# Kernel tuning notes

Measured on AMD Instinct MI355X. Metric: run time of the kernel, lower is better.

The kernel has to match this reference:

```python
import jax, jax.numpy as jnp
import numpy as np

B, T, C = 2, 4096, 512
H = 8
MEMORY = 256  # window: key j visible to query i iff 0 <= i - j <= MEMORY


def setup_inputs() -> dict:
    key = jax.random.key(0)
    k1, k2, k3 = jax.random.split(key, 3)
    x = jax.random.normal(k1, (B, T, C), dtype=jnp.float32)
    w_attn = jax.random.normal(k2, (3 * C, C), dtype=jnp.float32) * 0.02
    w_proj = jax.random.normal(k3, (C, C), dtype=jnp.float32) * 0.02
    return {"x": x, "w_attn": w_attn, "w_proj": w_proj}


def reference(x, w_attn, w_proj):
    b, t, c = x.shape
    d = c // H
    # fused QKV projection (Linear without bias): x @ W^T
    qkv = jnp.einsum('btc,fc->btf', x, w_attn)  # [B,T,3C]
    q, k, v = jnp.split(qkv, 3, axis=-1)
    # [B,T,C] -> [B,H,T,d]
    q = q.reshape(b, t, H, d).transpose(0, 2, 1, 3)
    k = k.reshape(b, t, H, d).transpose(0, 2, 1, 3)
    v = v.reshape(b, t, H, d).transpose(0, 2, 1, 3)
    # sliding-window causal mask: tril(0) & ~tril(-memory-1)
    i = jnp.arange(t)[:, None]
    j = jnp.arange(t)[None, :]
    mask = (j <= i) & (i - j <= MEMORY)  # [T,T] bool
    scores = jnp.einsum('bhqd,bhkd->bhqk', q, k) * (1.0 / np.sqrt(d))
    scores = jnp.where(mask, scores, -jnp.inf)
    attn = jax.nn.softmax(scores, axis=-1)
    y = jnp.einsum('bhqk,bhkd->bhqd', attn, v)  # [B,H,T,d]
    y = y.transpose(0, 2, 1, 3).reshape(b, t, c)
    # output projection
    y = jnp.einsum('btc,fc->btf', y, w_proj)
    return y
```

## Files before the change

### kernel.cpp

```cpp
#include <hip/hip_runtime.h>
#include <hip/hip_bf16.h>
#include <stdint.h>

#define BB 2
#define TT 4096
#define CC 512
#define HH 8
#define MEM 256

typedef unsigned short u16;
typedef __bf16 bf16x8 __attribute__((ext_vector_type(8)));
typedef float floatx4 __attribute__((ext_vector_type(4)));

__device__ inline u16 f2bf(float f) {
  uint32_t u = __float_as_uint(f);
  uint32_t r = (u + 0x7fffu + ((u >> 16) & 1u)) >> 16;
  return (u16)r;
}
__device__ inline u16 f2bf_r(float f) {
  return (u16)((__float_as_uint(f) + 0x8000u) >> 16);
}

__device__ inline void gld16(const u16* g, u16* lds) {
  __builtin_amdgcn_global_load_lds(
      (const __attribute__((address_space(1))) uint32_t*)g,
      (__attribute__((address_space(3))) uint32_t*)lds, 16, 0, 0);
}

#define BARM() asm volatile("" ::: "memory")

__global__ __launch_bounds__(256) void cvt_all(const float* __restrict__ x,
                                               const float* __restrict__ wa,
                                               const float* __restrict__ wp,
                                               u16* __restrict__ xb,
                                               u16* __restrict__ wab,
                                               u16* __restrict__ wpb) {
  int i = blockIdx.x * 256 + threadIdx.x;
  const float* s; u16* d; int off;
  if (i < 1048576) { s = x; d = xb; off = i; }
  else if (i < 1245184) { s = wa; d = wab; off = i - 1048576; }
  else { s = wp; d = wpb; off = i - 1245184; }
  float4 v = *reinterpret_cast<const float4*>(s + (size_t)off * 4);
  ushort4 o;
  o.x = f2bf(v.x); o.y = f2bf(v.y); o.z = f2bf(v.z); o.w = f2bf(v.w);
  *reinterpret_cast<ushort4*>(d + (size_t)off * 4) = o;
}

__device__ inline void stage_hA(const u16* __restrict__ G, u16* lds, int K,
                                int gr0, int koff, int half, int wv, int lane) {
#pragma unroll
  for (int j = 0; j < 2; j++) {
    int lrow = (j * 8 + wv) * 8 + (lane >> 3);
    int row = (lrow & 63) + ((lrow >> 6) << 7) + (half << 6);
    int blk = (lane & 7) ^ (row & 7);
    gld16(G + (size_t)(gr0 + row) * K + koff + blk * 8,
          lds + (size_t)row * 64 + (lane & 7) * 8);
  }
}
__device__ inline void stage_hB(const u16* __restrict__ G, u16* lds, int K,
                                int gr0, int koff, int half, int wv, int lane) {
  if (half == 0) {
#pragma unroll
    for (int j = 0; j < 2; j++) {
      int lrow = (j * 8 + wv) * 8 + (lane >> 3);
      int row = (lrow & 31) + (lrow >> 5) * 48;
      int blk = (lane & 7) ^ (row & 7);
      gld16(G + (size_t)(gr0 + row) * K + koff + blk * 8,
            lds + (size_t)row * 64 + (lane & 7) * 8);
    }
  } else {
    int lrow = wv * 8 + (lane >> 3);
    int row = 32 + (lrow & 15) + (lrow >> 4) * 48;
    int blk = (lane & 7) ^ (row & 7);
    gld16(G + (size_t)(gr0 + row) * K + koff + blk * 8,
          lds + (size_t)row * 64 + (lane & 7) * 8);
  }
}

#define PHASE(MQ, NQ, NF, STAGE, WAITV)                                        \
  {                                                                            \
    bf16x8 af[4][2], bfv[NF][2];                                               \
    _Pragma("unroll") for (int fm = 0; fm < 4; fm++) {                         \
      int row = wm * 128 + MQ * 64 + fm * 16 + l16;                            \
      const u16* p = Ad + (size_t)row * 64;                                    \
      af[fm][0] = *(const bf16x8*)(p + ((quad ^ (row & 7)) << 3));             \
      af[fm][1] = *(const bf16x8*)(p + (((4 + quad) ^ (row & 7)) << 3));       \
    }                                                                          \
    _Pragma("unroll") for (int fn = 0; fn < NF; fn++) {                        \
      int row = wn * 48 + NQ * 32 + fn * 16 + l16;                             \
      const u16* p = Bd + (size_t)row * 64;                                    \
      bfv[fn][0] = *(const bf16x8*)(p + ((quad ^ (row & 7)) << 3));            \
      bfv[fn][1] = *(const bf16x8*)(p + (((4 + quad) ^ (row & 7)) << 3));      \
    }                                                                          \
    STAGE;                                                                     \
    BARM();                                                                    \
    __builtin_amdgcn_s_barrier();                                              \
    asm volatile("s_waitcnt lgkmcnt(0)" ::: "memory");                         \
    __builtin_amdgcn_sched_barrier(0);                                         \
    __builtin_amdgcn_s_setprio(1);                                             \
    _Pragma("unroll") for (int fm = 0; fm < 4; fm++)                           \
      _Pragma("unroll") for (int fn = 0; fn < NF; fn++) {                      \
        acc[MQ * 4 + fm][NQ * 2 + fn] =                                        \
            __builtin_amdgcn_mfma_f32_16x16x32_bf16(                           \
                af[fm][0], bfv[fn][0], acc[MQ * 4 + fm][NQ * 2 + fn], 0, 0, 0);\
        acc[MQ * 4 + fm][NQ * 2 + fn] =                                        \
            __builtin_amdgcn_mfma_f32_16x16x32_bf16(                           \
                af[fm][1], bfv[fn][1], acc[MQ * 4 + fm][NQ * 2 + fn], 0, 0, 0);\
      }                                                                        \
    __builtin_amdgcn_s_setprio(0);                                             \
    WAITV;                                                                     \
    BARM();                                                                    \
    __builtin_amdgcn_s_barrier();                                              \
    BARM();                                                                    \
  }

__global__ __launch_bounds__(512, 2) void gemm256(const u16* __restrict__ A,
                                                  const u16* __restrict__ Bw,
                                                  u16* __restrict__ C,
                                                  int M, int N, int K) {
  __shared__ __align__(16) u16 As[2][256 * 64];
  __shared__ __align__(16) u16 Bs[2][192 * 64];
  const int tid = threadIdx.x;
  const int lane = tid & 63, wv = tid >> 6;
  const int quad = lane >> 4, l16 = lane & 15;
  const int wm = wv >> 2, wn = wv & 3;

  const int nbx = N / 192;
  const int nwg = (M >> 8) * nbx;
  int wg = blockIdx.x;
  if ((nwg & 7) == 0) wg = (wg & 7) * (nwg >> 3) + (wg >> 3);
  const int m0 = (wg / nbx) << 8, n0 = (wg % nbx) * 192;

  const int nK = K >> 6;
  floatx4 acc[8][3] = {};

  stage_hA(A, As[0], K, m0, 0, 0, wv, lane);
  stage_hA(A, As[0], K, m0, 0, 1, wv, lane);
  stage_hB(Bw, Bs[0], K, n0, 0, 0, wv, lane);
  stage_hB(Bw, Bs[0], K, n0, 0, 1, wv, lane);
  if (nK > 1) {
    stage_hA(A, As[1], K, m0, 64, 0, wv, lane);
    stage_hB(Bw, Bs[1], K, n0, 64, 0, wv, lane);
    asm volatile("s_waitcnt vmcnt(4)" ::: "memory");
  } else {
    asm volatile("s_waitcnt vmcnt(0)" ::: "memory");
  }
  BARM();
  __builtin_amdgcn_s_barrier();
  BARM();

  for (int t = 0; t < nK; ++t) {
    const int d = t & 1;
    u16* Ad = As[d]; u16* Bd = Bs[d];
    u16* An = As[d ^ 1]; u16* Bn = Bs[d ^ 1];
    const int k1 = (t + 1) << 6, k2 = (t + 2) << 6;

    PHASE(0, 0, 2, { if (t + 1 < nK) stage_hA(A, An, K, m0, k1, 1, wv, lane); }, {})
    PHASE(0, 1, 1, { if (t + 1 < nK) stage_hB(Bw, Bn, K, n0, k1, 1, wv, lane); }, {})
    PHASE(1, 0, 2, { if (t + 2 < nK) stage_hA(A, Ad, K, m0, k2, 0, wv, lane); }, {})
    PHASE(1, 1, 1, { if (t + 2 < nK) stage_hB(Bw, Bd, K, n0, k2, 0, wv, lane); },
          { if (t + 2 < nK) asm volatile("s_waitcnt vmcnt(4)" ::: "memory");
            else            asm volatile("s_waitcnt vmcnt(0)" ::: "memory"); })
  }

#pragma unroll
  for (int mi = 0; mi < 8; mi++) {
    int row = m0 + wm * 128 + mi * 16 + quad * 4;
#pragma unroll
    for (int ni = 0; ni < 3; ni++) {
      int col = n0 + wn * 48 + ni * 16 + l16;
#pragma unroll
      for (int r = 0; r < 4; r++)
        C[(size_t)(row + r) * N + col] = f2bf(acc[mi][ni][r]);
    }
  }
}

__global__ __launch_bounds__(256) void gemm_bt_n64(const u16* __restrict__ A,
                                                   const u16* __restrict__ Bw,
                                                   float* __restrict__ C,
                                                   int M, int N, int K) {
  __shared__ __align__(16) u16 As[128 * 32];
  __shared__ __align__(16) u16 Bs[64 * 32];
  const int tid = threadIdx.x;
  const int w = tid >> 6, lane = tid & 63, quad = lane >> 4, l16 = lane & 15;
  const int m0 = blockIdx.x * 128, n0 = blockIdx.y * 64;

  floatx4 acc[2][4] = {};
  const int nK = K >> 5;
  for (int kb = 0; kb < nK; ++kb) {
    const int kof = kb * 32;
    {
      int c = tid;
      gld16(A + (size_t)(m0 + (c >> 2)) * K + kof + (c & 3) * 8, As + (size_t)c * 8);
      c = tid + 256;
      gld16(A + (size_t)(m0 + (c >> 2)) * K + kof + (c & 3) * 8, As + (size_t)c * 8);
      c = tid;
      gld16(Bw + (size_t)(n0 + (c >> 2)) * K + kof + (c & 3) * 8, Bs + (size_t)c * 8);
    }
    __syncthreads();
    bf16x8 af[2], bfr[4];
#pragma unroll
    for (int i = 0; i < 2; i++)
      af[i] = *reinterpret_cast<const bf16x8*>(&As[(w * 32 + i * 16 + l16) * 32 + quad * 8]);
#pragma unroll
    for (int i = 0; i < 4; i++)
      bfr[i] = *reinterpret_cast<const bf16x8*>(&Bs[(i * 16 + l16) * 32 + quad * 8]);
#pragma unroll
    for (int mi = 0; mi < 2; mi++)
#pragma unroll
      for (int ni = 0; ni < 4; ni++)
        acc[mi][ni] = __builtin_amdgcn_mfma_f32_16x16x32_bf16(af[mi], bfr[ni], acc[mi][ni], 0, 0, 0);
    __syncthreads();
  }
#pragma unroll
  for (int mi = 0; mi < 2; mi++) {
    int row = m0 + w * 32 + mi * 16 + quad * 4;
#pragma unroll
    for (int ni = 0; ni < 4; ni++) {
      int col = n0 + ni * 16 + l16;
#pragma unroll
      for (int r = 0; r < 4; r++)
        C[(size_t)(row + r) * N + col] = acc[mi][ni][r];
    }
  }
}

__global__ __launch_bounds__(256, 2) void attn_win(const u16* __restrict__ qkv,
                                                   u16* __restrict__ y) {
  const int q0 = blockIdx.x * 128;
  const int h = blockIdx.y;
  const int b = blockIdx.z;
  const int tid = threadIdx.x;
  const int w = tid >> 6, lane = tid & 63, quad = lane >> 4, l16 = lane & 15;

  __shared__ __align__(16) u16 Qs[128 * 64];
  __shared__ __align__(16) u16 Ks[64 * 64];
  __shared__ __align__(16) u16 Vt[64 * 72];
  __shared__ __align__(16) u16 Ps[4][32 * 72];

  const size_t baseQ = ((size_t)(b * TT + q0)) * 1536 + h * 64;
#pragma unroll
  for (int j = 0; j < 4; j++) {
    int c = tid + j * 256, row = c >> 3, blk = (c & 7) ^ (row & 7);
    gld16(qkv + baseQ + (size_t)row * 1536 + blk * 8, Qs + (size_t)c * 8);
  }
  __syncthreads();
  bf16x8 qf[2][2];
#pragma unroll
  for (int mi = 0; mi < 2; mi++) {
    int row = w * 32 + mi * 16 + l16;
    qf[mi][0] = *reinterpret_cast<const bf16x8*>(&Qs[row * 64 + (quad ^ (l16 & 7)) * 8]);
    qf[mi][1] = *reinterpret_cast<const bf16x8*>(&Qs[row * 64 + ((quad + 4) ^ (l16 & 7)) * 8]);
#pragma unroll
    for (int e = 0; e < 8; e++) {
      qf[mi][0][e] = qf[mi][0][e] * (__bf16)0.125f;
      qf[mi][1][e] = qf[mi][1][e] * (__bf16)0.125f;
    }
  }

  floatx4 acc_o[2][4] = {};
  float l_acc[2][4] = {{0.f, 0.f, 0.f, 0.f}, {0.f, 0.f, 0.f, 0.f}};

  const int s_min = (q0 >= 256) ? 0 : ((256 - q0) >> 6);
  const int key_v = tid >> 3, dc_v = tid & 7;
  const int key_v1 = (tid + 256) >> 3, dc_v1 = tid & 7;

  uint4 vp0, vp1;
  {
    size_t baseV = ((size_t)(b * TT + (q0 - 256 + s_min * 64))) * 1536 + 1024 + h * 64;
    vp0 = *reinterpret_cast<const uint4*>(qkv + baseV + (size_t)key_v * 1536 + dc_v * 8);
    vp1 = *reinterpret_cast<const uint4*>(qkv + baseV + (size_t)key_v1 * 1536 + dc_v1 * 8);
  }

  for (int s = s_min; s < 6; ++s) {
    const int k0 = q0 - 256 + s * 64;
    const size_t baseK = ((size_t)(b * TT + k0)) * 1536 + 512 + h * 64;
    {
      int c = tid, row = c >> 3, blk = (c & 7) ^ (row & 7);
      gld16(qkv + baseK + (size_t)row * 1536 + blk * 8, Ks + (size_t)c * 8);
      c = tid + 256; row = c >> 3; blk = (c & 7) ^ (row & 7);
      gld16(qkv + baseK + (size_t)row * 1536 + blk * 8, Ks + (size_t)c * 8);
    }
    {
      u16 tmp[8];
      *reinterpret_cast<uint4*>(tmp) = vp0;
      int col = key_v ^ (dc_v * 8);
#pragma unroll
      for (int e = 0; e < 8; e++) Vt[(dc_v * 8 + e) * 72 + col] = tmp[e];
      *reinterpret_cast<uint4*>(tmp) = vp1;
      col = key_v1 ^ (dc_v1 * 8);
#pragma unroll
      for (int e = 0; e < 8; e++) Vt[(dc_v1 * 8 + e) * 72 + col] = tmp[e];
    }
    if (s < 5) {
      size_t baseV = ((size_t)(b * TT + k0 + 64)) * 1536 + 1024 + h * 64;
      vp0 = *reinterpret_cast<const uint4*>(qkv + baseV + (size_t)key_v * 1536 + dc_v * 8);
      vp1 = *reinterpret_cast<const uint4*>(qkv + baseV + (size_t)key_v1 * 1536 + dc_v1 * 8);
    }
    __syncthreads();

    int mode = 0;
    if (s == 0) mode = (w < 2) ? 1 : 3;
    else if (s == 1) mode = (w < 2) ? 0 : 1;
    else if (s == 4) mode = (w < 2) ? 2 : 0;
    else if (s == 5) mode = (w < 2) ? 3 : 2;

    if (mode != 3) {
      bf16x8 bfr[4][2];
#pragma unroll
      for (int nt = 0; nt < 4; nt++) {
        int krow = nt * 16 + l16;
        bfr[nt][0] = *reinterpret_cast<const bf16x8*>(&Ks[krow * 64 + (quad ^ (l16 & 7)) * 8]);
        bfr[nt][1] = *reinterpret_cast<const bf16x8*>(&Ks[krow * 64 + ((quad + 4) ^ (l16 & 7)) * 8]);
      }
      floatx4 sc[2][4] = {};
#pragma unroll
      for (int mi = 0; mi < 2; mi++)
#pragma unroll
        for (int nt = 0; nt < 4; nt++) {
          sc[mi][nt] = __builtin_amdgcn_mfma_f32_16x16x32_bf16(qf[mi][0], bfr[nt][0], sc[mi][nt], 0, 0, 0);
          sc[mi][nt] = __builtin_amdgcn_mfma_f32_16x16x32_bf16(qf[mi][1], bfr[nt][1], sc[mi][nt], 0, 0, 0);
        }
      const int hqb = (w & 1) * 32 + quad * 4;
      if (mode == 1) {
#pragma unroll
        for (int mi = 0; mi < 2; mi++)
#pragma unroll
          for (int nt = 0; nt < 4; nt++)
#pragma unroll
            for (int r = 0; r < 4; r++)
              if (hqb + mi * 16 + r > nt * 16 + l16) sc[mi][nt][r] = -1e30f;
      } else if (mode == 2) {
#pragma unroll
        for (int mi = 0; mi < 2; mi++)
#pragma unroll
          for (int nt = 0; nt < 4; nt++)
#pragma unroll
            for (int r = 0; r < 4; r++)
              if (hqb + mi * 16 + r < nt * 16 + l16) sc[mi][nt][r] = -1e30f;
      }
#pragma unroll
      for (int mi = 0; mi < 2; mi++)
#pragma unroll
        for (int nt = 0; nt < 4; nt++)
#pragma unroll
          for (int r = 0; r < 4; r++) {
            float p = __expf(sc[mi][nt][r] - 4.0f);
            l_acc[mi][r] += p;
            Ps[w][(mi * 16 + quad * 4 + r) * 72 + nt * 16 + l16] = f2bf_r(p);
          }
#pragma unroll
      for (int mi = 0; mi < 2; mi++)
#pragma unroll
        for (int ki = 0; ki < 2; ki++) {
          bf16x8 pf = *reinterpret_cast<const bf16x8*>(
              &Ps[w][(mi * 16 + l16) * 72 + ki * 32 + quad * 8]);
#pragma unroll
          for (int nt = 0; nt < 4; nt++) {
            int d = nt * 16 + l16;
            bf16x8 vf = *reinterpret_cast<const bf16x8*>(
                &Vt[d * 72 + ((ki * 32 + quad * 8) ^ (d & 56))]);
            acc_o[mi][nt] = __builtin_amdgcn_mfma_f32_16x16x32_bf16(pf, vf, acc_o[mi][nt], 0, 0, 0);
          }
        }
    }
    __syncthreads();
  }
#pragma unroll
  for (int mi = 0; mi < 2; mi++)
#pragma unroll
    for (int r = 0; r < 4; r++) {
      float l = l_acc[mi][r];
      l += __shfl_xor(l, 1);
      l += __shfl_xor(l, 2);
      l += __shfl_xor(l, 4);
      l += __shfl_xor(l, 8);
      float inv = 1.f / l;
      int row = q0 + w * 32 + mi * 16 + quad * 4 + r;
      size_t base = (size_t)(b * TT + row) * 512 + h * 64;
#pragma unroll
      for (int nt = 0; nt < 4; nt++)
        y[base + nt * 16 + l16] = f2bf(acc_o[mi][nt][r] * inv);
    }
}

extern "C" void kernel_launch(void* const* d_in, const int* in_sizes, int n_in,
                              void* d_out, int out_size, void* d_ws, size_t ws_size,
                              hipStream_t stream) {
  const float* x = (const float*)d_in[0];
  const float* w_attn = (const float*)d_in[1];
  const float* w_proj = (const float*)d_in[2];
  float* out = (float*)d_out;

  u16* xb = (u16*)d_ws;
  u16* wab = xb + (size_t)8192 * 512;
  u16* wpb = wab + (size_t)1536 * 512;
  u16* qkv = wpb + (size_t)512 * 512;
  u16* yb = qkv + (size_t)8192 * 1536;

  cvt_all<<<5120, 256, 0, stream>>>(x, w_attn, w_proj, xb, wab, wpb);
  gemm256<<<256, 512, 0, stream>>>(xb, wab, qkv, 8192, 1536, 512);
  attn_win<<<dim3(TT / 128, HH, BB), 256, 0, stream>>>(qkv, yb);
  gemm_bt_n64<<<dim3(64, 8), 256, 0, stream>>>(yb, wpb, out, 8192, 512, 512);
}
```

Before: 126.6 us.

## Fuse all four stages into one cooperative persistent kernel with grid syncs

Replaces four separate launches (convert, QKV GEMM, windowed attention, output projection) with a single cooperative kernel of 256 blocks of 512 threads, separated by grid.sync barriers. Each stage body is factored into a device function and remapped onto the fixed grid, with attention and projection running two sub-blocks per workgroup over shared LDS. The aim is to remove kernel launch gaps and inter-kernel drain. In exchange, grid barriers add cost, and stages such as attention and the projection now run with fewer concurrent blocks than their original launch grids. The old four-launch path is kept as a fallback if the cooperative launch fails.

Result: slower. 232.0 us (+83.2%).

```diff
diff --git a/kernel.cpp b/kernel.cpp
--- a/kernel.cpp
+++ b/kernel.cpp
@@ -1,6 +1,9 @@
 #include <hip/hip_runtime.h>
 #include <hip/hip_bf16.h>
+#include <hip/hip_cooperative_groups.h>
 #include <stdint.h>
+
+namespace cg = cooperative_groups;
 
 #define BB 2
 #define TT 4096
@@ -29,25 +32,28 @@
 
 #define BARM() asm volatile("" ::: "memory")
 
-__global__ __launch_bounds__(256) void cvt_all(const float* __restrict__ x,
-                                               const float* __restrict__ wa,
-                                               const float* __restrict__ wp,
-                                               u16* __restrict__ xb,
-                                               u16* __restrict__ wab,
-                                               u16* __restrict__ wpb) {
-  int i = blockIdx.x * 256 + threadIdx.x;
-  const float* s; u16* d; int off;
-  if (i < 1048576) { s = x; d = xb; off = i; }
-  else if (i < 1245184) { s = wa; d = wab; off = i - 1048576; }
-  else { s = wp; d = wpb; off = i - 1245184; }
-  float4 v = *reinterpret_cast<const float4*>(s + (size_t)off * 4);
-  ushort4 o;
-  o.x = f2bf(v.x); o.y = f2bf(v.y); o.z = f2bf(v.z); o.w = f2bf(v.w);
-  *reinterpret_cast<ushort4*>(d + (size_t)off * 4) = o;
-}
-
-__device__ inline void stage_hA(const u16* __restrict__ G, u16* lds, int K,
-                                int gr0, int koff, int half, int wv, int lane) {
+
+__device__ __forceinline__ void cvt_body(int gtid, int stride,
+                                         const float* __restrict__ x,
+                                         const float* __restrict__ wa,
+                                         const float* __restrict__ wp,
+                                         u16* __restrict__ xb,
+                                         u16* __restrict__ wab,
+                                         u16* __restrict__ wpb) {
+  for (int i = gtid; i < 1310720; i += stride) {
+    const float* s; u16* d; int off;
+    if (i < 1048576) { s = x; d = xb; off = i; }
+    else if (i < 1245184) { s = wa; d = wab; off = i - 1048576; }
+    else { s = wp; d = wpb; off = i - 1245184; }
+    float4 v = *reinterpret_cast<const float4*>(s + (size_t)off * 4);
+    ushort4 o;
+    o.x = f2bf(v.x); o.y = f2bf(v.y); o.z = f2bf(v.z); o.w = f2bf(v.w);
+    *reinterpret_cast<ushort4*>(d + (size_t)off * 4) = o;
+  }
+}
+
+__device__ __forceinline__ void stage_hA(const u16* __restrict__ G, u16* lds, int K,
+                                         int gr0, int koff, int half, int wv, int lane) {
 #pragma unroll
   for (int j = 0; j < 2; j++) {
     int lrow = (j * 8 + wv) * 8 + (lane >> 3);
@@ -57,8 +63,8 @@
           lds + (size_t)row * 64 + (lane & 7) * 8);
   }
 }
-__device__ inline void stage_hB(const u16* __restrict__ G, u16* lds, int K,
-                                int gr0, int koff, int half, int wv, int lane) {
+__device__ __forceinline__ void stage_hB(const u16* __restrict__ G, u16* lds, int K,
+                                         int gr0, int koff, int half, int wv, int lane) {
   if (half == 0) {
 #pragma unroll
     for (int j = 0; j < 2; j++) {
@@ -114,33 +120,35 @@
     BARM();                                                                    \
   }
 
-__global__ __launch_bounds__(512, 2) void gemm256(const u16* __restrict__ A,
-                                                  const u16* __restrict__ Bw,
-                                                  u16* __restrict__ C,
-                                                  int M, int N, int K) {
-  __shared__ __align__(16) u16 As[2][256 * 64];
-  __shared__ __align__(16) u16 Bs[2][192 * 64];
-  const int tid = threadIdx.x;
+__device__ __forceinline__ void gemm_body(const u16* __restrict__ A,
+                                          const u16* __restrict__ Bw,
+                                          u16* __restrict__ C,
+                                          int M, int N, int K,
+                                          u16* sm, int tid, int bx) {
+  u16* As0 = sm;
+  u16* As1 = sm + 16384;
+  u16* Bs0 = sm + 32768;
+  u16* Bs1 = sm + 45056;
   const int lane = tid & 63, wv = tid >> 6;
   const int quad = lane >> 4, l16 = lane & 15;
   const int wm = wv >> 2, wn = wv & 3;
 
   const int nbx = N / 192;
   const int nwg = (M >> 8) * nbx;
-  int wg = blockIdx.x;
+  int wg = bx;
   if ((nwg & 7) == 0) wg = (wg & 7) * (nwg >> 3) + (wg >> 3);
   const int m0 = (wg / nbx) << 8, n0 = (wg % nbx) * 192;
 
   const int nK = K >> 6;
   floatx4 acc[8][3] = {};
 
-  stage_hA(A, As[0], K, m0, 0, 0, wv, lane);
-  stage_hA(A, As[0], K, m0, 0, 1, wv, lane);
-  stage_hB(Bw, Bs[0], K, n0, 0, 0, wv, lane);
-  stage_hB(Bw, Bs[0], K, n0, 0, 1, wv, lane);
+  stage_hA(A, As0, K, m0, 0, 0, wv, lane);
+  stage_hA(A, As0, K, m0, 0, 1, wv, lane);
+  stage_hB(Bw, Bs0, K, n0, 0, 0, wv, lane);
+  stage_hB(Bw, Bs0, K, n0, 0, 1, wv, lane);
   if (nK > 1) {
-    stage_hA(A, As[1], K, m0, 64, 0, wv, lane);
-    stage_hB(Bw, Bs[1], K, n0, 64, 0, wv, lane);
+    stage_hA(A, As1, K, m0, 64, 0, wv, lane);
+    stage_hB(Bw, Bs1, K, n0, 64, 0, wv, lane);
     asm volatile("s_waitcnt vmcnt(4)" ::: "memory");
   } else {
     asm volatile("s_waitcnt vmcnt(0)" ::: "memory");
@@ -151,8 +159,8 @@
 
   for (int t = 0; t < nK; ++t) {
     const int d = t & 1;
-    u16* Ad = As[d]; u16* Bd = Bs[d];
-    u16* An = As[d ^ 1]; u16* Bn = Bs[d ^ 1];
+    u16* Ad = d ? As1 : As0; u16* Bd = d ? Bs1 : Bs0;
+    u16* An = d ? As0 : As1; u16* Bn = d ? Bs0 : Bs1;
     const int k1 = (t + 1) << 6, k2 = (t + 2) << 6;
 
     PHASE(0, 0, 2, { if (t + 1 < nK) stage_hA(A, An, K, m0, k1, 1, wv, lane); }, {})
@@ -176,73 +184,21 @@
   }
 }
 
-__global__ __launch_bounds__(256) void gemm_bt_n64(const u16* __restrict__ A,
-                                                   const u16* __restrict__ Bw,
-                                                   float* __restrict__ C,
-                                                   int M, int N, int K) {
-  __shared__ __align__(16) u16 As[128 * 32];
-  __shared__ __align__(16) u16 Bs[64 * 32];
-  const int tid = threadIdx.x;
-  const int w = tid >> 6, lane = tid & 63, quad = lane >> 4, l16 = lane & 15;
-  const int m0 = blockIdx.x * 128, n0 = blockIdx.y * 64;
-
-  floatx4 acc[2][4] = {};
-  const int nK = K >> 5;
-  for (int kb = 0; kb < nK; ++kb) {
-    const int kof = kb * 32;
-    {
-      int c = tid;
-      gld16(A + (size_t)(m0 + (c >> 2)) * K + kof + (c & 3) * 8, As + (size_t)c * 8);
-      c = tid + 256;
-      gld16(A + (size_t)(m0 + (c >> 2)) * K + kof + (c & 3) * 8, As + (size_t)c * 8);
-      c = tid;
-      gld16(Bw + (size_t)(n0 + (c >> 2)) * K + kof + (c & 3) * 8, Bs + (size_t)c * 8);
-    }
-    __syncthreads();
-    bf16x8 af[2], bfr[4];
-#pragma unroll
-    for (int i = 0; i < 2; i++)
-      af[i] = *reinterpret_cast<const bf16x8*>(&As[(w * 32 + i * 16 + l16) * 32 + quad * 8]);
-#pragma unroll
-    for (int i = 0; i < 4; i++)
-      bfr[i] = *reinterpret_cast<const bf16x8*>(&Bs[(i * 16 + l16) * 32 + quad * 8]);
-#pragma unroll
-    for (int mi = 0; mi < 2; mi++)
-#pragma unroll
-      for (int ni = 0; ni < 4; ni++)
-        acc[mi][ni] = __builtin_amdgcn_mfma_f32_16x16x32_bf16(af[mi], bfr[ni], acc[mi][ni], 0, 0, 0);
-    __syncthreads();
-  }
-#pragma unroll
-  for (int mi = 0; mi < 2; mi++) {
-    int row = m0 + w * 32 + mi * 16 + quad * 4;
-#pragma unroll
-    for (int ni = 0; ni < 4; ni++) {
-      int col = n0 + ni * 16 + l16;
-#pragma unroll
-      for (int r = 0; r < 4; r++)
-        C[(size_t)(row + r) * N + col] = acc[mi][ni][r];
-    }
-  }
-}
-
-__global__ __launch_bounds__(256, 2) void attn_win(const u16* __restrict__ qkv,
-                                                   u16* __restrict__ y) {
-  const int q0 = blockIdx.x * 128;
-  const int h = blockIdx.y;
-  const int b = blockIdx.z;
-  const int tid = threadIdx.x;
-  const int w = tid >> 6, lane = tid & 63, quad = lane >> 4, l16 = lane & 15;
-
-  __shared__ __align__(16) u16 Qs[128 * 64];
-  __shared__ __align__(16) u16 Ks[64 * 64];
-  __shared__ __align__(16) u16 Vt[64 * 72];
-  __shared__ __align__(16) u16 Ps[4][32 * 72];
+__device__ __forceinline__ void attn_body(const u16* __restrict__ qkv,
+                                          u16* __restrict__ y,
+                                          int q0, int h, int b, int t,
+                                          u16* base) {
+  u16* Qs = base;
+  u16* Ks = base + 8192;
+  u16* Vt = base + 12288;
+  u16* Ps0 = base + 16896;
+  const int w = t >> 6, lane = t & 63, quad = lane >> 4, l16 = lane & 15;
+  u16* Psw = Ps0 + w * 2304;
 
   const size_t baseQ = ((size_t)(b * TT + q0)) * 1536 + h * 64;
 #pragma unroll
   for (int j = 0; j < 4; j++) {
-    int c = tid + j * 256, row = c >> 3, blk = (c & 7) ^ (row & 7);
+    int c = t + j * 256, row = c >> 3, blk = (c & 7) ^ (row & 7);
     gld16(qkv + baseQ + (size_t)row * 1536 + blk * 8, Qs + (size_t)c * 8);
   }
   __syncthreads();
@@ -263,8 +219,8 @@
   float l_acc[2][4] = {{0.f, 0.f, 0.f, 0.f}, {0.f, 0.f, 0.f, 0.f}};
 
   const int s_min = (q0 >= 256) ? 0 : ((256 - q0) >> 6);
-  const int key_v = tid >> 3, dc_v = tid & 7;
-  const int key_v1 = (tid + 256) >> 3, dc_v1 = tid & 7;
+  const int key_v = t >> 3, dc_v = t & 7;
+  const int key_v1 = (t + 256) >> 3, dc_v1 = t & 7;
 
   uint4 vp0, vp1;
   {
@@ -277,9 +233,9 @@
     const int k0 = q0 - 256 + s * 64;
     const size_t baseK = ((size_t)(b * TT + k0)) * 1536 + 512 + h * 64;
     {
-      int c = tid, row = c >> 3, blk = (c & 7) ^ (row & 7);
+      int c = t, row = c >> 3, blk = (c & 7) ^ (row & 7);
       gld16(qkv + baseK + (size_t)row * 1536 + blk * 8, Ks + (size_t)c * 8);
-      c = tid + 256; row = c >> 3; blk = (c & 7) ^ (row & 7);
+      c = t + 256; row = c >> 3; blk = (c & 7) ^ (row & 7);
       gld16(qkv + baseK + (size_t)row * 1536 + blk * 8, Ks + (size_t)c * 8);
     }
     {
@@ -348,14 +304,14 @@
           for (int r = 0; r < 4; r++) {
             float p = __expf(sc[mi][nt][r] - 4.0f);
             l_acc[mi][r] += p;
-            Ps[w][(mi * 16 + quad * 4 + r) * 72 + nt * 16 + l16] = f2bf_r(p);
+            Psw[(mi * 16 + quad * 4 + r) * 72 + nt * 16 + l16] = f2bf_r(p);
           }
 #pragma unroll
       for (int mi = 0; mi < 2; mi++)
 #pragma unroll
         for (int ki = 0; ki < 2; ki++) {
           bf16x8 pf = *reinterpret_cast<const bf16x8*>(
-              &Ps[w][(mi * 16 + l16) * 72 + ki * 32 + quad * 8]);
+              &Psw[(mi * 16 + l16) * 72 + ki * 32 + quad * 8]);
 #pragma unroll
           for (int nt = 0; nt < 4; nt++) {
             int d = nt * 16 + l16;
@@ -378,11 +334,124 @@
       l += __shfl_xor(l, 8);
       float inv = 1.f / l;
       int row = q0 + w * 32 + mi * 16 + quad * 4 + r;
-      size_t base = (size_t)(b * TT + row) * 512 + h * 64;
+      size_t base2 = (size_t)(b * TT + row) * 512 + h * 64;
 #pragma unroll
       for (int nt = 0; nt < 4; nt++)
-        y[base + nt * 16 + l16] = f2bf(acc_o[mi][nt][r] * inv);
-    }
+        y[base2 + nt * 16 + l16] = f2bf(acc_o[mi][nt][r] * inv);
+    }
+}
+
+__device__ __forceinline__ void proj_body(const u16* __restrict__ A,
+                                          const u16* __restrict__ Bw,
+                                          float* __restrict__ C,
+                                          int m0, int n0, int t, u16* sm) {
+  u16* As = sm;
+  u16* Bs = sm + 4096;
+  const int w = t >> 6, lane = t & 63, quad = lane >> 4, l16 = lane & 15;
+  const int K = 512, N = 512;
+  floatx4 acc[2][4] = {};
+  for (int kb = 0; kb < 16; ++kb) {
+    const int kof = kb * 32;
+    {
+      int c = t;
+      gld16(A + (size_t)(m0 + (c >> 2)) * K + kof + (c & 3) * 8, As + (size_t)c * 8);
+      c = t + 256;
+      gld16(A + (size_t)(m0 + (c >> 2)) * K + kof + (c & 3) * 8, As + (size_t)c * 8);
+      c = t;
+      gld16(Bw + (size_t)(n0 + (c >> 2)) * K + kof + (c & 3) * 8, Bs + (size_t)c * 8);
+    }
+    __syncthreads();
+    bf16x8 af[2], bfr[4];
+#pragma unroll
+    for (int i = 0; i < 2; i++)
+      af[i] = *reinterpret_cast<const bf16x8*>(&As[(w * 32 + i * 16 + l16) * 32 + quad * 8]);
+#pragma unroll
+    for (int i = 0; i < 4; i++)
+      bfr[i] = *reinterpret_cast<const bf16x8*>(&Bs[(i * 16 + l16) * 32 + quad * 8]);
+#pragma unroll
+    for (int mi = 0; mi < 2; mi++)
+#pragma unroll
+      for (int ni = 0; ni < 4; ni++)
+        acc[mi][ni] = __builtin_amdgcn_mfma_f32_16x16x32_bf16(af[mi], bfr[ni], acc[mi][ni], 0, 0, 0);
+    __syncthreads();
+  }
+#pragma unroll
+  for (int mi = 0; mi < 2; mi++) {
+    int row = m0 + w * 32 + mi * 16 + quad * 4;
+#pragma unroll
+    for (int ni = 0; ni < 4; ni++) {
+      int col = n0 + ni * 16 + l16;
+#pragma unroll
+      for (int r = 0; r < 4; r++)
+        C[(size_t)(row + r) * N + col] = acc[mi][ni][r];
+    }
+  }
+}
+
+__global__ __launch_bounds__(512, 2) void mega(const float* __restrict__ x,
+                                               const float* __restrict__ wa,
+                                               const float* __restrict__ wp,
+                                               float* __restrict__ out,
+                                               u16* __restrict__ xb,
+                                               u16* __restrict__ wab,
+                                               u16* __restrict__ wpb,
+                                               u16* __restrict__ qkv,
+                                               u16* __restrict__ yb) {
+  __shared__ __align__(16) u16 sm[57344];
+  const int tid = threadIdx.x;
+  cg::grid_group grid = cg::this_grid();
+
+  cvt_body(blockIdx.x * 512 + tid, 256 * 512, x, wa, wp, xb, wab, wpb);
+  grid.sync();
+
+  gemm_body(xb, wab, qkv, 8192, 1536, 512, sm, tid, blockIdx.x);
+  grid.sync();
+
+  {
+    const int half = tid >> 8, t = tid & 255;
+    const int qt = blockIdx.x >> 3, pr = blockIdx.x & 7;
+    const int c = pr * 2 + half;
+    const int b = c >> 3, h = c & 7;
+    attn_body(qkv, yb, qt * 128, h, b, t, sm + half * 26112);
+  }
+  grid.sync();
+
+  {
+    const int half = tid >> 8, t = tid & 255;
+    const int m0 = (blockIdx.x >> 2) * 128;
+    const int n0 = (blockIdx.x & 3) * 128 + half * 64;
+    proj_body(yb, wpb, out, m0, n0, t, sm + half * 6144);
+  }
+}
+
+__global__ __launch_bounds__(256) void cvt_all(const float* __restrict__ x,
+                                               const float* __restrict__ wa,
+                                               const float* __restrict__ wp,
+                                               u16* __restrict__ xb,
+                                               u16* __restrict__ wab,
+                                               u16* __restrict__ wpb) {
+  cvt_body(blockIdx.x * 256 + threadIdx.x, gridDim.x * 256, x, wa, wp, xb, wab, wpb);
+}
+
+__global__ __launch_bounds__(512, 2) void gemm256(const u16* __restrict__ A,
+                                                  const u16* __restrict__ Bw,
+                                                  u16* __restrict__ C,
+                                                  int M, int N, int K) {
+  __shared__ __align__(16) u16 sm[57344];
+  gemm_body(A, Bw, C, M, N, K, sm, threadIdx.x, blockIdx.x);
+}
+
+__global__ __launch_bounds__(256, 2) void attn_win(const u16* __restrict__ qkv,
+                                                   u16* __restrict__ y) {
+  __shared__ __align__(16) u16 sm[26112];
+  attn_body(qkv, y, blockIdx.x * 128, blockIdx.y, blockIdx.z, threadIdx.x, sm);
+}
+
+__global__ __launch_bounds__(256) void gemm_bt_n64(const u16* __restrict__ A,
+                                                   const u16* __restrict__ Bw,
+                                                   float* __restrict__ C) {
+  __shared__ __align__(16) u16 sm[6144];
+  proj_body(A, Bw, C, blockIdx.x * 128, blockIdx.y * 64, threadIdx.x, sm);
 }
 
 extern "C" void kernel_launch(void* const* d_in, const int* in_sizes, int n_in,
@@ -399,8 +468,14 @@
   u16* qkv = wpb + (size_t)512 * 512;
   u16* yb = qkv + (size_t)8192 * 1536;
 
-  cvt_all<<<5120, 256, 0, stream>>>(x, w_attn, w_proj, xb, wab, wpb);
-  gemm256<<<256, 512, 0, stream>>>(xb, wab, qkv, 8192, 1536, 512);
-  attn_win<<<dim3(TT / 128, HH, BB), 256, 0, stream>>>(qkv, yb);
-  gemm_bt_n64<<<dim3(64, 8), 256, 0, stream>>>(yb, wpb, out, 8192, 512, 512);
-}
+  void* args[] = {(void*)&x, (void*)&w_attn, (void*)&w_proj, (void*)&out,
+                  (void*)&xb, (void*)&wab, (void*)&wpb, (void*)&qkv, (void*)&yb};
+  hipError_t rc = hipLaunchCooperativeKernel((const void*)mega, dim3(256), dim3(512),
+                                             args, 0, stream);
+  if (rc != hipSuccess) {
+    cvt_all<<<5120, 256, 0, stream>>>(x, w_attn, w_proj, xb, wab, wpb);
+    gemm256<<<256, 512, 0, stream>>>(xb, wab, qkv, 8192, 1536, 512);
+    attn_win<<<dim3(TT / 128, HH, BB), 256, 0, stream>>>(qkv, yb);
+    gemm_bt_n64<<<dim3(64, 8), 256, 0, stream>>>(yb, wpb, out);
+  }
+}
```
